# Kernel tuning notes

Measured on AMD Instinct MI355X. Metric: run time of the kernel, lower is better.

The kernel has to match this reference:

```python
import jax, jax.numpy as jnp
import numpy as np

B, S, H = 2, 1024, 2048
NH, NKV, HD = 16, 4, 128
KB = 1024
THETA = 10000.0
NREP = NH // NKV
NEG = -1e9


def rotate_half(x):
    x1, x2 = x[..., : HD // 2], x[..., HD // 2 :]
    return jnp.concatenate((-x2, x1), axis=-1)


def setup_inputs() -> dict:
    key = jax.random.key(0)
    ks = jax.random.split(key, 9)
    wscale = 1.0 / np.sqrt(H)
    hidden_states = jax.random.normal(ks[0], (B, S, H), dtype=jnp.float32)
    # causal additive mask over the self-attention block only
    causal = jnp.tril(jnp.ones((S, S), dtype=bool))
    attention_mask = jnp.where(causal, 0.0, NEG).astype(jnp.float32)
    attention_mask = jnp.broadcast_to(attention_mask[None, None], (B, 1, S, S))
    position_ids = jnp.broadcast_to(jnp.arange(S, dtype=jnp.int32)[None], (B, S))
    kb_keys = jax.random.normal(ks[1], (B, KB, NKV * HD), dtype=jnp.float32)
    kb_values = jax.random.normal(ks[2], (B, KB, NKV * HD), dtype=jnp.float32)
    Wq = jax.random.normal(ks[3], (NH * HD, H), dtype=jnp.float32) * wscale
    Wq_new = jax.random.normal(ks[4], (NH * HD, H), dtype=jnp.float32) * wscale
    Wk = jax.random.normal(ks[5], (NKV * HD, H), dtype=jnp.float32) * wscale
    Wv = jax.random.normal(ks[6], (NKV * HD, H), dtype=jnp.float32) * wscale
    Wo = jax.random.normal(ks[7], (H, NH * HD), dtype=jnp.float32) * wscale
    return {
        'hidden_states': hidden_states, 'attention_mask': attention_mask,
        'position_ids': position_ids, 'kb_keys': kb_keys, 'kb_values': kb_values,
        'Wq': Wq, 'Wq_new': Wq_new, 'Wk': Wk, 'Wv': Wv, 'Wo': Wo,
    }


def _rope(position_ids, dtype):
    inv_freq = 1.0 / (THETA ** (jnp.arange(0, HD, 2, dtype=jnp.float32) / HD))
    freqs = position_ids.astype(jnp.float32)[:, :, None] * inv_freq[None, None, :]  # (B,S,HD/2)
    emb = jnp.concatenate((freqs, freqs), axis=-1)  # (B,S,HD)
    return jnp.cos(emb).astype(dtype)[:, None], jnp.sin(emb).astype(dtype)[:, None]  # (B,1,S,HD)


def reference(hidden_states, attention_mask, position_ids, kb_keys, kb_values,
              Wq, Wq_new, Wk, Wv, Wo):
    x = hidden_states
    q = jnp.einsum('bsh,dh->bsd', x, Wq).reshape(B, S, NH, HD).transpose(0, 2, 1, 3)
    q_new = jnp.einsum('bsh,dh->bsd', x, Wq_new).reshape(B, S, NH, HD).transpose(0, 2, 1, 3)
    k = jnp.einsum('bsh,dh->bsd', x, Wk).reshape(B, S, NKV, HD).transpose(0, 2, 1, 3)
    v = jnp.einsum('bsh,dh->bsd', x, Wv).reshape(B, S, NKV, HD).transpose(0, 2, 1, 3)

    cos, sin = _rope(position_ids, x.dtype)
    q = q * cos + rotate_half(q) * sin          # roped self queries
    k = k * cos + rotate_half(k) * sin          # roped self keys; q_new / KB keys stay un-roped

    # GQA repeat of KV heads
    k = jnp.repeat(k, NREP, axis=1)             # (B,NH,S,HD)
    v = jnp.repeat(v, NREP, axis=1)
    kb_k = jnp.repeat(kb_keys.reshape(B, KB, NKV, HD).transpose(0, 2, 1, 3), NREP, axis=1)   # (B,NH,KB,HD)
    kb_v = jnp.repeat(kb_values.reshape(B, KB, NKV, HD).transpose(0, 2, 1, 3), NREP, axis=1)

    scale = 1.0 / np.sqrt(HD)
    scores_kb = jnp.einsum('bhqd,bhkd->bhqk', q_new, kb_k) * scale      # (B,NH,S,KB)
    scores_self = jnp.einsum('bhqd,bhkd->bhqk', q, k) * scale + attention_mask  # (B,NH,S,S)
    scores = jnp.concatenate((scores_kb, scores_self), axis=-1)          # (B,NH,S,KB+S)
    attn = jax.nn.softmax(scores, axis=-1)

    v_full = jnp.concatenate((kb_v, v), axis=2)                          # (B,NH,KB+S,HD)
    out = jnp.einsum('bhqk,bhkd->bhqd', attn, v_full)                    # (B,NH,S,HD)
    out = out.transpose(0, 2, 1, 3).reshape(B, S, NH * HD)
    return jnp.einsum('bsd,hd->bsh', out, Wo)
```

## Files before the change

### kernel.cpp

```cpp
#include <hip/hip_runtime.h>

#define Bc   2
#define Sc   1024
#define Hc   2048
#define NHc  16
#define NKVc 4
#define HDc  128
#define KBc  1024
#define NREPc 4

typedef unsigned short ushort_t;
typedef unsigned int uint32;
typedef __attribute__((ext_vector_type(8))) __bf16 bf16x8;
typedef __attribute__((ext_vector_type(4))) float f32x4;

static __device__ __forceinline__ size_t dsz(int x) { return (size_t)x; }

static __device__ __forceinline__ ushort_t f2bf(float f) {
  uint32 u = __float_as_uint(f);
  u += 0x7fffu + ((u >> 16) & 1u);
  return (ushort_t)(u >> 16);
}
static __device__ __forceinline__ float bf2f(ushort_t u) {
  return __uint_as_float(((uint32)u) << 16);
}

#define ROPE_INV 0.14391156831212787f
#define QSCALE   (0.08838834764831845f * 1.4426950408889634f)

#define FSEG 1048576
__global__ void conv_all(const float* __restrict__ x,  const float* __restrict__ Wq,
                         const float* __restrict__ Wqn, const float* __restrict__ Wk,
                         const float* __restrict__ Wv,  const float* __restrict__ Wo,
                         ushort_t* xb, ushort_t* Wqb, ushort_t* Wqnb,
                         ushort_t* Wkb, ushort_t* Wvb, ushort_t* Wob)
{
  int i = blockIdx.x * 256 + threadIdx.x;
  const float* s; ushort_t* d; int off;
  if      (i <     FSEG)            { s = x;   d = xb;   off = i; }
  else if (i < 2 * FSEG)            { s = Wq;  d = Wqb;  off = i - FSEG; }
  else if (i < 3 * FSEG)            { s = Wqn; d = Wqnb; off = i - 2 * FSEG; }
  else if (i < 3 * FSEG + FSEG / 4) { s = Wk;  d = Wkb;  off = i - 3 * FSEG; }
  else if (i < 3 * FSEG + FSEG / 2) { s = Wv;  d = Wvb;  off = i - 3 * FSEG - FSEG / 4; }
  else                              { s = Wo;  d = Wob;  off = i - 3 * FSEG - FSEG / 2; }
  float4 v = ((const float4*)s)[off];
  ushort4 o;
  o.x = f2bf(v.x); o.y = f2bf(v.y); o.z = f2bf(v.z); o.w = f2bf(v.w);
  ((ushort4*)d)[off] = o;
}

#define GL16(gsrc, ldst)                                                \
  __builtin_amdgcn_global_load_lds(                                     \
      (const __attribute__((address_space(1))) void*)(gsrc),            \
      (__attribute__((address_space(3))) void*)(ldst), 16, 0, 0)

__global__ __launch_bounds__(256) void gemm_proj(
    const ushort_t* __restrict__ A,
    const ushort_t* __restrict__ Wqb,  const ushort_t* __restrict__ Wqnb,
    const ushort_t* __restrict__ Wkb,  const ushort_t* __restrict__ Wvb,
    ushort_t* __restrict__ qb, ushort_t* __restrict__ qnb,
    ushort_t* __restrict__ kkvb, ushort_t* __restrict__ vkvb)
{
  __shared__ ushort_t sA[128 * 32];
  __shared__ ushort_t sB[128 * 32];

  const int K = Hc;
  const int bx = blockIdx.x;
  const ushort_t* Bseg; ushort_t* Cseg; int segN, colseg; float scale;
  if      (bx < 16) { Bseg = Wqb;  Cseg = qb;   segN = 2048; colseg = bx * 128;        scale = 1.f; }
  else if (bx < 32) { Bseg = Wqnb; Cseg = qnb;  segN = 2048; colseg = (bx - 16) * 128; scale = QSCALE; }
  else if (bx < 36) { Bseg = Wkb;  Cseg = kkvb; segN = 512;  colseg = (bx - 32) * 128; scale = 1.f; }
  else              { Bseg = Wvb;  Cseg = vkvb; segN = 512;  colseg = (bx - 36) * 128; scale = 1.f; }

  const int tid  = threadIdx.x;
  const int lane = tid & 63;
  const int wid  = tid >> 6;
  const int wr   = wid >> 1;
  const int wc   = wid & 1;
  const int row0 = blockIdx.y * 128;
  const int fr = lane & 15;
  const int fq = lane >> 4;

  f32x4 acc[4][4];
  #pragma unroll
  for (int m = 0; m < 4; ++m)
    #pragma unroll
    for (int n = 0; n < 4; ++n) acc[m][n] = (f32x4){0.f, 0.f, 0.f, 0.f};

  const int rS = tid >> 2;
  const int kg = (tid & 3) * 8;
  const ushort_t* Asrc0 = A + dsz(row0 + rS) * K + kg;
  const ushort_t* Asrc1 = A + dsz(row0 + 64 + rS) * K + kg;
  const ushort_t* Bsrc0 = Bseg + dsz(colseg + rS) * K + kg;
  const ushort_t* Bsrc1 = Bseg + dsz(colseg + 64 + rS) * K + kg;
  char* ldsA0 = (char*)sA + tid * 16;
  char* ldsA1 = (char*)sA + 4096 + tid * 16;
  char* ldsB0 = (char*)sB + tid * 16;
  char* ldsB1 = (char*)sB + 4096 + tid * 16;

  for (int k0 = 0; k0 < K; k0 += 32) {
    GL16(Asrc0 + k0, ldsA0);
    GL16(Asrc1 + k0, ldsA1);
    GL16(Bsrc0 + k0, ldsB0);
    GL16(Bsrc1 + k0, ldsB1);
    __syncthreads();

    bf16x8 a[4], b[4];
    #pragma unroll
    for (int m = 0; m < 4; ++m)
      a[m] = *(const bf16x8*)&sA[(wr * 64 + m * 16 + fr) * 32 + fq * 8];
    #pragma unroll
    for (int n = 0; n < 4; ++n)
      b[n] = *(const bf16x8*)&sB[(wc * 64 + n * 16 + fr) * 32 + fq * 8];
    #pragma unroll
    for (int m = 0; m < 4; ++m)
      #pragma unroll
      for (int n = 0; n < 4; ++n)
        acc[m][n] = __builtin_amdgcn_mfma_f32_16x16x32_bf16(a[m], b[n], acc[m][n], 0, 0, 0);
    __syncthreads();
  }

  #pragma unroll
  for (int m = 0; m < 4; ++m)
    #pragma unroll
    for (int n = 0; n < 4; ++n)
      #pragma unroll
      for (int j = 0; j < 4; ++j)
        Cseg[dsz(row0 + wr * 64 + m * 16 + fq * 4 + j) * segN +
             colseg + wc * 64 + n * 16 + fr] = f2bf(acc[m][n][j] * scale);
}

__global__ __launch_bounds__(256) void gemm_bt_bf16(
    const ushort_t* __restrict__ A, const ushort_t* __restrict__ B,
    float* __restrict__ C, int M, int N, int K)
{
  __shared__ ushort_t sA[128 * 32];
  __shared__ ushort_t sB[128 * 32];

  const int tid  = threadIdx.x;
  const int lane = tid & 63;
  const int wid  = tid >> 6;
  const int wr   = wid >> 1;
  const int wc   = wid & 1;
  const int row0 = blockIdx.y * 128;
  const int col0 = blockIdx.x * 128;
  const int fr = lane & 15;
  const int fq = lane >> 4;

  f32x4 acc[4][4];
  #pragma unroll
  for (int m = 0; m < 4; ++m)
    #pragma unroll
    for (int n = 0; n < 4; ++n) acc[m][n] = (f32x4){0.f, 0.f, 0.f, 0.f};

  const int rS = tid >> 2;
  const int kg = (tid & 3) * 8;
  const ushort_t* Asrc0 = A + dsz(row0 + rS) * K + kg;
  const ushort_t* Asrc1 = A + dsz(row0 + 64 + rS) * K + kg;
  const ushort_t* Bsrc0 = B + dsz(col0 + rS) * K + kg;
  const ushort_t* Bsrc1 = B + dsz(col0 + 64 + rS) * K + kg;
  char* ldsA0 = (char*)sA + tid * 16;
  char* ldsA1 = (char*)sA + 4096 + tid * 16;
  char* ldsB0 = (char*)sB + tid * 16;
  char* ldsB1 = (char*)sB + 4096 + tid * 16;

  for (int k0 = 0; k0 < K; k0 += 32) {
    GL16(Asrc0 + k0, ldsA0);
    GL16(Asrc1 + k0, ldsA1);
    GL16(Bsrc0 + k0, ldsB0);
    GL16(Bsrc1 + k0, ldsB1);
    __syncthreads();

    bf16x8 a[4], b[4];
    #pragma unroll
    for (int m = 0; m < 4; ++m)
      a[m] = *(const bf16x8*)&sA[(wr * 64 + m * 16 + fr) * 32 + fq * 8];
    #pragma unroll
    for (int n = 0; n < 4; ++n)
      b[n] = *(const bf16x8*)&sB[(wc * 64 + n * 16 + fr) * 32 + fq * 8];
    #pragma unroll
    for (int m = 0; m < 4; ++m)
      #pragma unroll
      for (int n = 0; n < 4; ++n)
        acc[m][n] = __builtin_amdgcn_mfma_f32_16x16x32_bf16(a[m], b[n], acc[m][n], 0, 0, 0);
    __syncthreads();
  }

  #pragma unroll
  for (int m = 0; m < 4; ++m)
    #pragma unroll
    for (int n = 0; n < 4; ++n)
      #pragma unroll
      for (int j = 0; j < 4; ++j)
        C[dsz(row0 + wr * 64 + m * 16 + fq * 4 + j) * N +
          col0 + wc * 64 + n * 16 + fr] = acc[m][n][j];
}

__global__ void rope_q_ip(ushort_t* __restrict__ qb, const int* __restrict__ pos)
{
  int idx = blockIdx.x * blockDim.x + threadIdx.x;
  int j = idx & 63;
  int h = (idx >> 6) & 15;
  int r = idx >> 10;
  float p = (float)pos[r];
  float f = p * expf(-(float)j * ROPE_INV);
  float c = cosf(f), s = sinf(f);
  ushort_t* d = qb + dsz(r) * (NHc * HDc) + h * HDc;
  float x1 = bf2f(d[j]), x2 = bf2f(d[j + 64]);
  d[j]      = f2bf((x1 * c - x2 * s) * QSCALE);
  d[j + 64] = f2bf((x2 * c + x1 * s) * QSCALE);
}

__global__ void rope_k_kcat(const ushort_t* __restrict__ kkvb, const int* __restrict__ pos,
                            ushort_t* __restrict__ Kcat)
{
  int idx = blockIdx.x * blockDim.x + threadIdx.x;
  int j = idx & 63;
  int kvh = (idx >> 6) & 3;
  int s = (idx >> 8) & 1023;
  int b = idx >> 18;
  float p = (float)pos[b * Sc + s];
  float f = p * expf(-(float)j * ROPE_INV);
  float c = cosf(f), sn = sinf(f);
  const ushort_t* src = kkvb + dsz(b * Sc + s) * (NKVc * HDc) + kvh * HDc;
  ushort_t* dst = Kcat + (dsz(b * NKVc + kvh) * 2048 + 1024 + s) * HDc;
  float x1 = bf2f(src[j]), x2 = bf2f(src[j + 64]);
  dst[j]      = f2bf(x1 * c - x2 * sn);
  dst[j + 64] = f2bf(x2 * c + x1 * sn);
}

__global__ void kb_kcat(const float* __restrict__ src, ushort_t* __restrict__ Kcat)
{
  int i = blockIdx.x * blockDim.x + threadIdx.x;
  int d4 = i & 31;
  int kvh = (i >> 5) & 3;
  int k = (i >> 7) & 1023;
  int b = i >> 17;
  float4 v = *(const float4*)&src[dsz(b * KBc + k) * (NKVc * HDc) + kvh * HDc + d4 * 4];
  ushort4 o;
  o.x = f2bf(v.x); o.y = f2bf(v.y); o.z = f2bf(v.z); o.w = f2bf(v.w);
  *(ushort4*)&Kcat[(dsz(b * NKVc + kvh) * 2048 + k) * HDc + d4 * 4] = o;
}

__global__ __launch_bounds__(256) void vt_build(const float* __restrict__ kbv,
                                                const ushort_t* __restrict__ vkvb,
                                                ushort_t* __restrict__ Vt)
{
  __shared__ float sT[32][33];
  const int k0 = blockIdx.x * 32;
  const int d0 = blockIdx.y * 32;
  const int bk = blockIdx.z;
  const int b = bk >> 2, kvh = bk & 3;
  const int tid = threadIdx.x;

  #pragma unroll
  for (int t = 0; t < 4; ++t) {
    int li = tid + t * 256;
    int kk = li >> 5, dl = li & 31;
    int kg = k0 + kk;
    float v = (kg < 1024)
      ? kbv[dsz(b * KBc + kg) * (NKVc * HDc) + kvh * HDc + d0 + dl]
      : bf2f(vkvb[dsz(b * Sc + kg - 1024) * (NKVc * HDc) + kvh * HDc + d0 + dl]);
    sT[kk][dl] = v;
  }
  __syncthreads();
  #pragma unroll
  for (int t = 0; t < 4; ++t) {
    int li = tid + t * 256;
    int dl = li >> 5, kk = li & 31;
    Vt[(dsz(b * NKVc + kvh) * HDc + d0 + dl) * 2048 + k0 + kk] = f2bf(sT[kk][dl]);
  }
}

__global__ __launch_bounds__(256, 4) void attn_mfma5(
    const ushort_t* __restrict__ Qr,
    const ushort_t* __restrict__ Qn,
    const ushort_t* __restrict__ Kcat,
    const ushort_t* __restrict__ Vt,
    ushort_t* __restrict__ Opart,
    float* __restrict__ mlpart)
{
  __shared__ ushort_t sK[2][32 * 128];
  __shared__ ushort_t sV[2][128 * 32];

  const int tid = threadIdx.x;
  const int lane = tid & 63;
  const int w = tid >> 6;
  const int fr = lane & 15;
  const int fq = lane >> 4;
  const int blk = blockIdx.x;
  const int half = blockIdx.y;
  const int qt = blk & 15;
  const int h  = (blk >> 4) & 15;
  const int b  = blk >> 8;
  const int kvh = h >> 2;
  const int qrow = qt * 64 + w * 16 + fr;
  const int kperm = ((fr >> 2) << 3) + (fr & 3);

  const ushort_t* Kb = Kcat + dsz(b * NKVc + kvh) * 2048 * HDc;
  const ushort_t* Vb = Vt   + dsz(b * NKVc + kvh) * HDc * 2048;

  const int nt  = 34 + 2 * qt;
  const int mid = nt >> 1;
  const int t_lo = half ? mid : 0;
  const int t_hi = half ? nt  : mid;

  const int kr0 = tid >> 4;
  const int ks0 = tid & 15;
  const int ku0 = (kr0 & 3) | ((kr0 >> 3) << 2);
  const int kOffA = kr0 * 256 + ((ks0 ^ ku0) * 16);
  const int kOffB = (kr0 + 16) * 256 + ((ks0 ^ (ku0 + 8)) * 16);
  const int vr0 = tid >> 2;
  const int vs0 = tid & 3;
  const int vu0 = (vr0 >> 1) & 3;
  const size_t vOffA = (size_t)vr0 * 4096 + ((vs0 ^ vu0) * 16);
  const size_t vOffB = vOffA + (size_t)64 * 4096;

  const int vslot = (fq ^ ((fr >> 1) & 3)) * 8;

#define STAGE(bi, t)                                                   \
  {                                                                    \
    const char* kgb = (const char*)Kb + (size_t)(t) * 8192;            \
    const char* vgb = (const char*)Vb + (size_t)(t) * 64;              \
    GL16(kgb + kOffA, (char*)&sK[bi][0] + tid * 16);                   \
    GL16(kgb + kOffB, (char*)&sK[bi][0] + 4096 + tid * 16);            \
    GL16(vgb + vOffA, (char*)&sV[bi][0] + tid * 16);                   \
    GL16(vgb + vOffB, (char*)&sV[bi][0] + 4096 + tid * 16);            \
  }

  bf16x8 qf[4];
  {
    const ushort_t* qp = (t_lo >= 32 ? Qr : Qn) + dsz(b * Sc + qrow) * (NHc * HDc) + h * HDc;
    #pragma unroll
    for (int c = 0; c < 4; ++c) qf[c] = *(const bf16x8*)&qp[c * 32 + fq * 8];
  }

  float m = -1e30f, l = 0.f;
  f32x4 ot[8];
  #pragma unroll
  for (int dt = 0; dt < 8; ++dt) ot[dt] = (f32x4){0.f, 0.f, 0.f, 0.f};

  STAGE(0, t_lo);
  __syncthreads();

  for (int t = t_lo; t < t_hi; ++t) {
    const int cur = (t - t_lo) & 1;
    if (t + 1 < t_hi) STAGE(cur ^ 1, t + 1);

    if (t == 32) {
      const ushort_t* qp = Qr + dsz(b * Sc + qrow) * (NHc * HDc) + h * HDc;
      #pragma unroll
      for (int c = 0; c < 4; ++c) qf[c] = *(const bf16x8*)&qp[c * 32 + fq * 8];
    }
    const bool self = (t >= 32);

    bf16x8 ka0[4], ka1[4], va[8];
    #pragma unroll
    for (int c = 0; c < 4; ++c) {
      const int ks = ((c * 4 + fq) ^ fr) * 8;
      ka0[c] = *(const bf16x8*)&sK[cur][kperm * 128 + ks];
      ka1[c] = *(const bf16x8*)&sK[cur][(kperm + 4) * 128 + ks];
    }
    #pragma unroll
    for (int dt = 0; dt < 8; ++dt)
      va[dt] = *(const bf16x8*)&sV[cur][(dt * 16 + fr) * 32 + vslot];

    f32x4 s0 = (f32x4){0.f, 0.f, 0.f, 0.f};
    f32x4 s1 = (f32x4){0.f, 0.f, 0.f, 0.f};
    #pragma unroll
    for (int c = 0; c < 4; ++c)
      s0 = __builtin_amdgcn_mfma_f32_16x16x32_bf16(ka0[c], qf[c], s0, 0, 0, 0);
    #pragma unroll
    for (int c = 0; c < 4; ++c)
      s1 = __builtin_amdgcn_mfma_f32_16x16x32_bf16(ka1[c], qf[c], s1, 0, 0, 0);

    if (self) {
      #pragma unroll
      for (int j = 0; j < 4; ++j) {
        s0[j] = (t * 32 + fq * 8 + j     - 1024 > qrow) ? -1e30f : s0[j];
        s1[j] = (t * 32 + fq * 8 + 4 + j - 1024 > qrow) ? -1e30f : s1[j];
      }
    }
    float tmax = fmaxf(fmaxf(fmaxf(s0[0], s0[1]), fmaxf(s0[2], s0[3])),
                       fmaxf(fmaxf(s1[0], s1[1]), fmaxf(s1[2], s1[3])));
    tmax = fmaxf(tmax, __shfl_xor(tmax, 16));
    tmax = fmaxf(tmax, __shfl_xor(tmax, 32));

    if (__any(tmax > m + 8.f)) {
      float mnew = fmaxf(m, tmax);
      float corr = exp2f(m - mnew);
      l *= corr;
      #pragma unroll
      for (int dt = 0; dt < 8; ++dt) {
        ot[dt][0] *= corr; ot[dt][1] *= corr;
        ot[dt][2] *= corr; ot[dt][3] *= corr;
      }
      m = mnew;
    }
    float ps = 0.f;
    bf16x8 pb;
    #pragma unroll
    for (int j = 0; j < 4; ++j) { float p = exp2f(s0[j] - m); ps += p; pb[j] = (__bf16)p; }
    #pragma unroll
    for (int j = 0; j < 4; ++j) { float p = exp2f(s1[j] - m); ps += p; pb[j + 4] = (__bf16)p; }
    l += ps;

    #pragma unroll
    for (int dt = 0; dt < 8; ++dt)
      ot[dt] = __builtin_amdgcn_mfma_f32_16x16x32_bf16(va[dt], pb, ot[dt], 0, 0, 0);

    __syncthreads();
  }
#undef STAGE

  l += __shfl_xor(l, 16);
  l += __shfl_xor(l, 32);

  const int qin = w * 16 + fr;
  ushort_t* ob = Opart + (dsz(half * 512 + blk) * 64 + qin) * 128;
  #pragma unroll
  for (int dt = 0; dt < 8; ++dt) {
    ushort_t o4a[4];
    #pragma unroll
    for (int j = 0; j < 4; ++j) o4a[j] = f2bf(ot[dt][j]);
    *(ushort4*)&ob[dt * 16 + fq * 4] = *(ushort4*)o4a;
  }
  if (fq == 0) {
    float* mlp = mlpart + (dsz(half * 512 + blk) * 64 + qin) * 2;
    mlp[0] = m;
    mlp[1] = l;
  }
}

__global__ void attn_merge(const ushort_t* __restrict__ Opart,
                           const float* __restrict__ mlpart,
                           ushort_t* __restrict__ attnb)
{
  const int i = blockIdx.x * 256 + threadIdx.x;
  const int e = i * 8;
  const int qg = e >> 7;
  const int d0 = e & 127;
  const int blk = qg >> 6;
  const int qin = qg & 63;
  const int qt = blk & 15;
  const int h  = (blk >> 4) & 15;
  const int b  = blk >> 8;

  const float* ml0 = mlpart + dsz(blk) * 128 + qin * 2;
  const float* ml1 = mlpart + dsz(512 + blk) * 128 + qin * 2;
  const float m0 = ml0[0], l0 = ml0[1];
  const float m1 = ml1[0], l1 = ml1[1];
  const float M = fmaxf(m0, m1);
  const float s0 = exp2f(m0 - M), s1 = exp2f(m1 - M);
  const float Linv = 1.f / (l0 * s0 + l1 * s1);
  const float c0 = s0 * Linv, c1 = s1 * Linv;

  const ushort_t* o0 = Opart + (dsz(blk) * 64 + qin) * 128 + d0;
  const ushort_t* o1 = Opart + (dsz(512 + blk) * 64 + qin) * 128 + d0;
  ushort4 a0 = *(const ushort4*)&o0[0];
  ushort4 b0 = *(const ushort4*)&o1[0];
  ushort4 a1 = *(const ushort4*)&o0[4];
  ushort4 b1 = *(const ushort4*)&o1[4];

  ushort_t r[8];
  r[0] = f2bf(bf2f(a0.x) * c0 + bf2f(b0.x) * c1);
  r[1] = f2bf(bf2f(a0.y) * c0 + bf2f(b0.y) * c1);
  r[2] = f2bf(bf2f(a0.z) * c0 + bf2f(b0.z) * c1);
  r[3] = f2bf(bf2f(a0.w) * c0 + bf2f(b0.w) * c1);
  r[4] = f2bf(bf2f(a1.x) * c0 + bf2f(b1.x) * c1);
  r[5] = f2bf(bf2f(a1.y) * c0 + bf2f(b1.y) * c1);
  r[6] = f2bf(bf2f(a1.z) * c0 + bf2f(b1.z) * c1);
  r[7] = f2bf(bf2f(a1.w) * c0 + bf2f(b1.w) * c1);

  ushort_t* dst = attnb + dsz(b * Sc + qt * 64 + qin) * (NHc * HDc) + h * HDc + d0;
  *(ushort4*)&dst[0] = *(ushort4*)&r[0];
  *(ushort4*)&dst[4] = *(ushort4*)&r[4];
}

extern "C" void kernel_launch(void* const* d_in, const int* in_sizes, int n_in,
                              void* d_out, int out_size, void* d_ws, size_t ws_size,
                              hipStream_t stream)
{
  const float* x    = (const float*)d_in[0];
  const int*   pos  = (const int*)d_in[2];
  const float* kbk  = (const float*)d_in[3];
  const float* kbv  = (const float*)d_in[4];
  const float* Wq   = (const float*)d_in[5];
  const float* Wqn  = (const float*)d_in[6];
  const float* Wk   = (const float*)d_in[7];
  const float* Wv   = (const float*)d_in[8];
  const float* Wo   = (const float*)d_in[9];
  float* out = (float*)d_out;

  const int MR = Bc * Sc;
  const size_t MU = 1048576;

  ushort_t* U = (ushort_t*)d_ws;
  ushort_t* xb    = U;
  ushort_t* Wqb   = U + 4  * MU;
  ushort_t* Wqnb  = U + 8  * MU;
  ushort_t* Wkb   = U + 12 * MU;
  ushort_t* Wvb   = U + 13 * MU;
  ushort_t* Wob   = U + 14 * MU;
  ushort_t* qb    = U + 18 * MU;
  ushort_t* qnb   = U + 22 * MU;
  ushort_t* kkvb  = U + 26 * MU;
  ushort_t* vkvb  = U + 27 * MU;
  ushort_t* Kcat  = U + 28 * MU;
  ushort_t* Vt    = U + 30 * MU;
  ushort_t* attnb = U + 32 * MU;
  ushort_t* Opart  = U;
  float*    mlpart = (float*)(U + 26 * MU);

  dim3 blk(256);

  conv_all<<<18432, blk, 0, stream>>>(x, Wq, Wqn, Wk, Wv, Wo,
                                      xb, Wqb, Wqnb, Wkb, Wvb, Wob);
  gemm_proj<<<dim3(40, 16), blk, 0, stream>>>(xb, Wqb, Wqnb, Wkb, Wvb,
                                              qb, qnb, kkvb, vkvb);
  rope_q_ip<<<8192, blk, 0, stream>>>(qb, pos);
  kb_kcat<<<1024, blk, 0, stream>>>(kbk, Kcat);
  rope_k_kcat<<<2048, blk, 0, stream>>>(kkvb, pos, Kcat);
  vt_build<<<dim3(64, 4, 8), blk, 0, stream>>>(kbv, vkvb, Vt);
  attn_mfma5<<<dim3(512, 2), blk, 0, stream>>>(qb, qnb, Kcat, Vt, Opart, mlpart);
  attn_merge<<<2048, blk, 0, stream>>>(Opart, mlpart, attnb);
  gemm_bt_bf16<<<dim3(16, 16), blk, 0, stream>>>(attnb, Wob, out, MR, 2048, Hc);
}
```

Baseline: 198.3 us.

## Use 128-row query tiles with 512 threads and three-way KV split

Measured after the change: 433.4 us. 2.19x slower.

```diff
diff --git a/kernel.cpp b/kernel.cpp
--- a/kernel.cpp
+++ b/kernel.cpp
@@ -272,7 +272,7 @@
   }
 }
 
-__global__ __launch_bounds__(256, 4) void attn_mfma5(
+__global__ __launch_bounds__(512, 6) void attn_mfma6(
     const ushort_t* __restrict__ Qr,
     const ushort_t* __restrict__ Qn,
     const ushort_t* __restrict__ Kcat,
@@ -289,32 +289,29 @@
   const int fr = lane & 15;
   const int fq = lane >> 4;
   const int blk = blockIdx.x;
-  const int half = blockIdx.y;
-  const int qt = blk & 15;
-  const int h  = (blk >> 4) & 15;
-  const int b  = blk >> 8;
+  const int third = blockIdx.y;
+  const int qt = blk & 7;
+  const int h  = (blk >> 3) & 15;
+  const int b  = blk >> 7;
   const int kvh = h >> 2;
-  const int qrow = qt * 64 + w * 16 + fr;
+  const int qrow = qt * 128 + w * 16 + fr;
   const int kperm = ((fr >> 2) << 3) + (fr & 3);
 
   const ushort_t* Kb = Kcat + dsz(b * NKVc + kvh) * 2048 * HDc;
   const ushort_t* Vb = Vt   + dsz(b * NKVc + kvh) * HDc * 2048;
 
-  const int nt  = 34 + 2 * qt;
-  const int mid = nt >> 1;
-  const int t_lo = half ? mid : 0;
-  const int t_hi = half ? nt  : mid;
-
-  const int kr0 = tid >> 4;
-  const int ks0 = tid & 15;
-  const int ku0 = (kr0 & 3) | ((kr0 >> 3) << 2);
-  const int kOffA = kr0 * 256 + ((ks0 ^ ku0) * 16);
-  const int kOffB = (kr0 + 16) * 256 + ((ks0 ^ (ku0 + 8)) * 16);
-  const int vr0 = tid >> 2;
-  const int vs0 = tid & 3;
-  const int vu0 = (vr0 >> 1) & 3;
-  const size_t vOffA = (size_t)vr0 * 4096 + ((vs0 ^ vu0) * 16);
-  const size_t vOffB = vOffA + (size_t)64 * 4096;
+  const int nt  = 36 + 4 * qt;
+  const int q3 = nt / 3, r3 = nt % 3;
+  const int t_lo = third * q3 + (third < r3 ? third : r3);
+  const int t_hi = t_lo + q3 + (third < r3 ? 1 : 0);
+
+  const int krr = tid >> 4;
+  const int kss = tid & 15;
+  const int kuu = (krr & 3) | ((krr >> 3) << 2);
+  const int kOff = krr * 256 + ((kss ^ kuu) * 16);
+  const int vrr = tid >> 2;
+  const int vss = tid & 3;
+  const size_t vOff = (size_t)vrr * 4096 + (((vss ^ ((vrr >> 1) & 3))) * 16);
 
   const int vslot = (fq ^ ((fr >> 1) & 3)) * 8;
 
@@ -322,10 +319,8 @@
   {                                                                    \
     const char* kgb = (const char*)Kb + (size_t)(t) * 8192;            \
     const char* vgb = (const char*)Vb + (size_t)(t) * 64;              \
-    GL16(kgb + kOffA, (char*)&sK[bi][0] + tid * 16);                   \
-    GL16(kgb + kOffB, (char*)&sK[bi][0] + 4096 + tid * 16);            \
-    GL16(vgb + vOffA, (char*)&sV[bi][0] + tid * 16);                   \
-    GL16(vgb + vOffB, (char*)&sV[bi][0] + 4096 + tid * 16);            \
+    GL16(kgb + kOff, (char*)&sK[bi][0] + tid * 16);                    \
+    GL16(vgb + vOff, (char*)&sV[bi][0] + tid * 16);                    \
   }
 
   bf16x8 qf[4];
@@ -417,7 +412,7 @@
   l += __shfl_xor(l, 32);
 
   const int qin = w * 16 + fr;
-  ushort_t* ob = Opart + (dsz(half * 512 + blk) * 64 + qin) * 128;
+  ushort_t* ob = Opart + (dsz(third * 256 + blk) * 128 + qin) * 128;
   #pragma unroll
   for (int dt = 0; dt < 8; ++dt) {
     ushort_t o4a[4];
@@ -426,7 +421,7 @@
     *(ushort4*)&ob[dt * 16 + fq * 4] = *(ushort4*)o4a;
   }
   if (fq == 0) {
-    float* mlp = mlpart + (dsz(half * 512 + blk) * 64 + qin) * 2;
+    float* mlp = mlpart + (dsz(third * 256 + blk) * 128 + qin) * 2;
     mlp[0] = m;
     mlp[1] = l;
   }
@@ -440,39 +435,44 @@
   const int e = i * 8;
   const int qg = e >> 7;
   const int d0 = e & 127;
-  const int blk = qg >> 6;
-  const int qin = qg & 63;
-  const int qt = blk & 15;
-  const int h  = (blk >> 4) & 15;
-  const int b  = blk >> 8;
-
-  const float* ml0 = mlpart + dsz(blk) * 128 + qin * 2;
-  const float* ml1 = mlpart + dsz(512 + blk) * 128 + qin * 2;
-  const float m0 = ml0[0], l0 = ml0[1];
-  const float m1 = ml1[0], l1 = ml1[1];
-  const float M = fmaxf(m0, m1);
-  const float s0 = exp2f(m0 - M), s1 = exp2f(m1 - M);
-  const float Linv = 1.f / (l0 * s0 + l1 * s1);
-  const float c0 = s0 * Linv, c1 = s1 * Linv;
-
-  const ushort_t* o0 = Opart + (dsz(blk) * 64 + qin) * 128 + d0;
-  const ushort_t* o1 = Opart + (dsz(512 + blk) * 64 + qin) * 128 + d0;
-  ushort4 a0 = *(const ushort4*)&o0[0];
-  ushort4 b0 = *(const ushort4*)&o1[0];
-  ushort4 a1 = *(const ushort4*)&o0[4];
-  ushort4 b1 = *(const ushort4*)&o1[4];
+  const int blk = qg >> 7;
+  const int qin = qg & 127;
+  const int qt = blk & 7;
+  const int h  = (blk >> 3) & 15;
+  const int b  = blk >> 7;
+
+  float mm[3], ll[3];
+  #pragma unroll
+  for (int p = 0; p < 3; ++p) {
+    const float* ml = mlpart + (dsz(p * 256 + blk) * 128 + qin) * 2;
+    mm[p] = ml[0]; ll[p] = ml[1];
+  }
+  float M = fmaxf(fmaxf(mm[0], mm[1]), mm[2]);
+  float sc[3], L = 0.f;
+  #pragma unroll
+  for (int p = 0; p < 3; ++p) { sc[p] = exp2f(mm[p] - M); L += ll[p] * sc[p]; }
+  const float Linv = 1.f / L;
+  #pragma unroll
+  for (int p = 0; p < 3; ++p) sc[p] *= Linv;
+
+  float acc[8];
+  #pragma unroll
+  for (int j = 0; j < 8; ++j) acc[j] = 0.f;
+  #pragma unroll
+  for (int p = 0; p < 3; ++p) {
+    const ushort_t* o = Opart + (dsz(p * 256 + blk) * 128 + qin) * 128 + d0;
+    ushort4 a0 = *(const ushort4*)&o[0];
+    ushort4 a1 = *(const ushort4*)&o[4];
+    acc[0] += bf2f(a0.x) * sc[p]; acc[1] += bf2f(a0.y) * sc[p];
+    acc[2] += bf2f(a0.z) * sc[p]; acc[3] += bf2f(a0.w) * sc[p];
+    acc[4] += bf2f(a1.x) * sc[p]; acc[5] += bf2f(a1.y) * sc[p];
+    acc[6] += bf2f(a1.z) * sc[p]; acc[7] += bf2f(a1.w) * sc[p];
+  }
 
   ushort_t r[8];
-  r[0] = f2bf(bf2f(a0.x) * c0 + bf2f(b0.x) * c1);
-  r[1] = f2bf(bf2f(a0.y) * c0 + bf2f(b0.y) * c1);
-  r[2] = f2bf(bf2f(a0.z) * c0 + bf2f(b0.z) * c1);
-  r[3] = f2bf(bf2f(a0.w) * c0 + bf2f(b0.w) * c1);
-  r[4] = f2bf(bf2f(a1.x) * c0 + bf2f(b1.x) * c1);
-  r[5] = f2bf(bf2f(a1.y) * c0 + bf2f(b1.y) * c1);
-  r[6] = f2bf(bf2f(a1.z) * c0 + bf2f(b1.z) * c1);
-  r[7] = f2bf(bf2f(a1.w) * c0 + bf2f(b1.w) * c1);
-
-  ushort_t* dst = attnb + dsz(b * Sc + qt * 64 + qin) * (NHc * HDc) + h * HDc + d0;
+  #pragma unroll
+  for (int j = 0; j < 8; ++j) r[j] = f2bf(acc[j]);
+  ushort_t* dst = attnb + dsz(b * Sc + qt * 128 + qin) * (NHc * HDc) + h * HDc + d0;
   *(ushort4*)&dst[0] = *(ushort4*)&r[0];
   *(ushort4*)&dst[4] = *(ushort4*)&r[4];
 }
@@ -522,7 +522,7 @@
   kb_kcat<<<1024, blk, 0, stream>>>(kbk, Kcat);
   rope_k_kcat<<<2048, blk, 0, stream>>>(kkvb, pos, Kcat);
   vt_build<<<dim3(64, 4, 8), blk, 0, stream>>>(kbv, vkvb, Vt);
-  attn_mfma5<<<dim3(512, 2), blk, 0, stream>>>(qb, qnb, Kcat, Vt, Opart, mlpart);
+  attn_mfma6<<<dim3(256, 3), dim3(512), 0, stream>>>(qb, qnb, Kcat, Vt, Opart, mlpart);
   attn_merge<<<2048, blk, 0, stream>>>(Opart, mlpart, attnb);
   gemm_bt_bf16<<<dim3(16, 16), blk, 0, stream>>>(attnb, Wob, out, MR, 2048, Hc);
 }
```
